# Kernel optimization log

Measured on AMD Instinct MI355X. Metric: run time of the kernel, lower is better.

The kernel has to match this reference:

```python
import jax, jax.numpy as jnp
import numpy as np

GRID_LO = 32
GRID_HI = 128
NF = 4          # n_features
K = 9           # num_neighbors
NUM_CLASSES = 36
BS = 128
P_LO = GRID_LO * GRID_LO   # 1024
P_HI = GRID_HI * GRID_HI   # 16384


def _knn_neighbor_indices():
    """Replicates cKDTree(lo_coords).query(hi_coords, k=K)[1]: lo grid has
    spacing ratio=grid_hi//grid_lo, hi grid spacing 1; neighbors sorted by
    distance (stable sort -> ties broken by lower linear index)."""
    ratio = GRID_HI // GRID_LO
    lo = np.stack(np.meshgrid(np.arange(GRID_LO) * ratio,
                              np.arange(GRID_LO) * ratio, indexing='ij'),
                  axis=-1).reshape(-1, 2).astype(np.float64)   # (P_LO, 2)
    hi = np.stack(np.meshgrid(np.arange(GRID_HI),
                              np.arange(GRID_HI), indexing='ij'),
                  axis=-1).reshape(-1, 2).astype(np.float64)   # (P_HI, 2)
    d2 = ((hi[:, None, :] - lo[None, :, :]) ** 2).sum(-1)      # (P_HI, P_LO)
    idx = np.argsort(d2, axis=1, kind='stable')[:, :K]          # (P_HI, K)
    return jnp.asarray(idx, dtype=jnp.int32)


def setup_inputs() -> dict:
    key = jax.random.key(0)
    k1, k2, k3, k4, k5 = jax.random.split(key, 5)
    x = jax.random.normal(k1, (BS, NF * P_LO), dtype=jnp.float32)
    cls_ids = jax.random.randint(k2, (BS,), 0, NUM_CLASSES)
    neighbor_indices = _knn_neighbor_indices()                  # (P_HI, K)
    weight_map = jax.random.normal(k3, (NUM_CLASSES, NF, P_HI, K), dtype=jnp.float32) * 0.05
    bias_low = jax.random.normal(k4, (NUM_CLASSES, NF, P_LO), dtype=jnp.float32) * 0.05
    bias_high = jax.random.normal(k5, (NUM_CLASSES, NF, P_HI), dtype=jnp.float32) * 0.05
    return {"x": x, "cls_ids": cls_ids, "neighbor_indices": neighbor_indices,
            "weight_map": weight_map, "bias_low": bias_low, "bias_high": bias_high}


def reference(x, cls_ids, neighbor_indices, weight_map, bias_low, bias_high):
    # x: (BS, NF*P_LO) -> (BS, NF, P_LO)
    y_low = x.reshape(x.shape[0], NF, P_LO)
    y_low_db = y_low - bias_low[cls_ids]                        # (BS, NF, P_LO)
    # gather k=9 lo-res neighbors for every hi-res pixel (all features at once)
    neigh = y_low_db[:, :, neighbor_indices]                    # (BS, NF, P_HI, K)
    weights = weight_map[cls_ids]                               # (BS, NF, P_HI, K)
    out = jnp.einsum('bfpk,bfpk->bfp', neigh, weights)          # weighted sum over k
    out = out + bias_high[cls_ids]                              # (BS, NF, P_HI)
    return out.reshape(x.shape[0], NF, GRID_HI, GRID_HI)
```

## Files before the change

### kernel.cpp

```cpp
#include <hip/hip_runtime.h>

#define BS      128
#define NF      4
#define NC      36
#define P_LO    1024
#define P_HI    16384
#define KNN     9
#define THREADS 256
#define TILE_P  256
#define NTILES  (P_HI / TILE_P)
#define LIST_OFF 64
#define SCHED_OFF 36

#define WBUF_BYTES (TILE_P * KNN * 4)
#define YBUF_BYTES (P_LO * 16)

__global__ __launch_bounds__(128) void build_lists_kernel(
    const int* __restrict__ cls_ids, int* __restrict__ ws)
{
    __shared__ int cnt[NC];
    __shared__ int pk[9];
    const int t = threadIdx.x;
    if (t < NC) cnt[t] = 0;
    if (t >= 64 && t < 73) pk[t - 64] = 0;
    __syncthreads();
    if (t < BS) {
        int c = cls_ids[t];
        int pos = atomicAdd(&cnt[c], 1);
        ws[LIST_OFF + c * BS + pos] = t;
    }
    __syncthreads();
    if (t < NC) {
        int ct = cnt[t];
        ws[t] = ct;
        int r = 0;
        for (int j = 0; j < NC; ++j) {
            int cj = cnt[j];
            r += (cj > ct) || (cj == ct && j < t);
        }
        atomicOr(&pk[r >> 2], t << ((r & 3) << 3));
    }
    __syncthreads();
    if (t < 9) ws[SCHED_OFF + t] = pk[t];
}

__device__ __forceinline__ void async_cp16(const void* g, void* l) {
    __builtin_amdgcn_global_load_lds(
        (const __attribute__((address_space(1))) void*)g,
        (__attribute__((address_space(3))) void*)l, 16, 0, 0);
}

__global__ __launch_bounds__(THREADS) void rect_up_kernel(
    const float* __restrict__ x,
    const int*   __restrict__ ws,
    const int*   __restrict__ nbr,
    const float* __restrict__ wmap,
    const float* __restrict__ blo,
    const float* __restrict__ bhi,
    float*       __restrict__ out)
{
    __shared__ __align__(16) char smem[WBUF_BYTES + YBUF_BYTES];

    const int tile = blockIdx.x & (NTILES - 1);
    const int g    = blockIdx.x >> 6;
    const int cls  = (ws[SCHED_OFF + (g >> 2)] >> ((g & 3) << 3)) & 0xFF;

    const int n_b = ws[cls];
    if (n_b == 0) return;

    const int tid   = threadIdx.x;
    const int tbase = tile * TILE_P;
    const int p     = tbase + tid;

    float4* wbuf  = (float4*)smem;
    float4* ybuf4 = (float4*)(smem + WBUF_BYTES);
    float4* idst  = ybuf4;

    {
        const float4* wsrc = (const float4*)(wmap + ((size_t)(cls * NF + 0) * P_HI + tbase) * KNN);
        const float4* isrc = (const float4*)(nbr + (size_t)tbase * KNN);
        async_cp16(wsrc + tid,       wbuf + tid);
        async_cp16(wsrc + tid + 256, wbuf + tid + 256);
        async_cp16(isrc + tid,       idst + tid);
        async_cp16(isrc + tid + 256, idst + tid + 256);
        if (tid < 64) {
            async_cp16(wsrc + 512 + tid, wbuf + 512 + tid);
            async_cp16(isrc + 512 + tid, idst + 512 + tid);
        }
    }

    const int* list = ws + LIST_OFF + cls * BS;
    const int bid0 = list[0];
    const int bid1 = (1 < n_b) ? list[1] : bid0;
    const int bid2 = (2 < n_b) ? list[2] : bid0;
    const int bid3 = (3 < n_b) ? list[3] : bid0;

    float xv[16];
    {
        const float* x0 = x + ((size_t)(bid0 * NF + 0)) * P_LO;
        const float* x1 = x + ((size_t)(bid1 * NF + 0)) * P_LO;
        const float* x2 = x + ((size_t)(bid2 * NF + 0)) * P_LO;
        const float* x3 = x + ((size_t)(bid3 * NF + 0)) * P_LO;
        #pragma unroll
        for (int m = 0; m < 4; ++m) {
            const int q = tid + (m << 8);
            xv[m * 4 + 0] = x0[q];
            xv[m * 4 + 1] = x1[q];
            xv[m * 4 + 2] = x2[q];
            xv[m * 4 + 3] = x3[q];
        }
    }

    asm volatile("s_waitcnt vmcnt(0)" ::: "memory");
    __syncthreads();

    int nb[KNN];
    {
        const int* irow = (const int*)(smem + WBUF_BYTES) + (size_t)tid * KNN;
        #pragma unroll
        for (int k = 0; k < KNN; ++k) nb[k] = irow[k];
    }

    const int R = (n_b + 3) >> 2;

    for (int f = 0; f < NF; ++f) {
        float blv[4];
        {
            const float* blp = blo + (size_t)(cls * NF + f) * P_LO;
            #pragma unroll
            for (int m = 0; m < 4; ++m) blv[m] = blp[tid + (m << 8)];
        }
        const float bh = bhi[(size_t)(cls * NF + f) * P_HI + p];

        float w[KNN];
        {
            const float* wrow = (const float*)smem + (size_t)tid * KNN;
            #pragma unroll
            for (int k = 0; k < KNN; ++k) w[k] = wrow[k];
        }
        __syncthreads();

        for (int r = 0; r < R; ++r) {
            int c0, c1, c2, c3;
            if (r == 0) {
                c0 = bid0; c1 = bid1; c2 = bid2; c3 = bid3;
                #pragma unroll
                for (int m = 0; m < 4; ++m) {
                    float4 v;
                    v.x = xv[m * 4 + 0] - blv[m];
                    v.y = xv[m * 4 + 1] - blv[m];
                    v.z = xv[m * 4 + 2] - blv[m];
                    v.w = xv[m * 4 + 3] - blv[m];
                    ybuf4[tid + (m << 8)] = v;
                }
            } else {
                const int s0 = 4 * r;
                c0 = list[s0];
                c1 = (s0 + 1 < n_b) ? list[s0 + 1] : c0;
                c2 = (s0 + 2 < n_b) ? list[s0 + 2] : c0;
                c3 = (s0 + 3 < n_b) ? list[s0 + 3] : c0;
                const float* x0 = x + ((size_t)(c0 * NF + f)) * P_LO;
                const float* x1 = x + ((size_t)(c1 * NF + f)) * P_LO;
                const float* x2 = x + ((size_t)(c2 * NF + f)) * P_LO;
                const float* x3 = x + ((size_t)(c3 * NF + f)) * P_LO;
                #pragma unroll
                for (int m = 0; m < 4; ++m) {
                    const int q = tid + (m << 8);
                    float4 v;
                    v.x = x0[q] - blv[m];
                    v.y = x1[q] - blv[m];
                    v.z = x2[q] - blv[m];
                    v.w = x3[q] - blv[m];
                    ybuf4[q] = v;
                }
            }
            __syncthreads();

            if (r == 0 && f + 1 < NF) {
                const float4* wsrc = (const float4*)(wmap + ((size_t)(cls * NF + f + 1) * P_HI + tbase) * KNN);
                async_cp16(wsrc + tid,       wbuf + tid);
                async_cp16(wsrc + tid + 256, wbuf + tid + 256);
                if (tid < 64) async_cp16(wsrc + 512 + tid, wbuf + 512 + tid);
                const float* x0 = x + ((size_t)(bid0 * NF + f + 1)) * P_LO;
                const float* x1 = x + ((size_t)(bid1 * NF + f + 1)) * P_LO;
                const float* x2 = x + ((size_t)(bid2 * NF + f + 1)) * P_LO;
                const float* x3 = x + ((size_t)(bid3 * NF + f + 1)) * P_LO;
                #pragma unroll
                for (int m = 0; m < 4; ++m) {
                    const int q = tid + (m << 8);
                    xv[m * 4 + 0] = x0[q];
                    xv[m * 4 + 1] = x1[q];
                    xv[m * 4 + 2] = x2[q];
                    xv[m * 4 + 3] = x3[q];
                }
            }

            float a0 = 0.f, a1 = 0.f, a2 = 0.f, a3 = 0.f;
            #pragma unroll
            for (int k = 0; k < KNN; ++k) {
                const float4 yv = ybuf4[nb[k]];
                a0 = fmaf(w[k], yv.x, a0);
                a1 = fmaf(w[k], yv.y, a1);
                a2 = fmaf(w[k], yv.z, a2);
                a3 = fmaf(w[k], yv.w, a3);
            }
            const int s0 = 4 * r;
            out[(size_t)(c0 * NF + f) * P_HI + p] = a0 + bh;
            if (s0 + 1 < n_b) out[(size_t)(c1 * NF + f) * P_HI + p] = a1 + bh;
            if (s0 + 2 < n_b) out[(size_t)(c2 * NF + f) * P_HI + p] = a2 + bh;
            if (s0 + 3 < n_b) out[(size_t)(c3 * NF + f) * P_HI + p] = a3 + bh;

            if (r + 1 < R) __syncthreads();
        }
        if (f + 1 < NF) __syncthreads();
    }
}

extern "C" void kernel_launch(void* const* d_in, const int* in_sizes, int n_in,
                              void* d_out, int out_size, void* d_ws, size_t ws_size,
                              hipStream_t stream) {
    const float* x    = (const float*)d_in[0];
    const int*   cls  = (const int*)d_in[1];
    const int*   nbr  = (const int*)d_in[2];
    const float* wmap = (const float*)d_in[3];
    const float* blo  = (const float*)d_in[4];
    const float* bhi  = (const float*)d_in[5];
    float*       out  = (float*)d_out;
    int*         wsl  = (int*)d_ws;

    build_lists_kernel<<<1, 128, 0, stream>>>(cls, wsl);
    rect_up_kernel<<<NC * NTILES, THREADS, 0, stream>>>(
        x, wsl, nbr, wmap, blo, bhi, out);
}
```

Baseline: 163.8 us.

## Split features across blocks and prefetch next batch group during compute

The grid grows so that each block handles a single feature instead of looping over all four. Weights and neighbor indices now come straight from global memory into registers, replacing the async LDS copies. Inside the batch-group loop, x for the next group is loaded into registers before the current gather runs, and barriers wait only on lgkmcnt rather than doing a full syncthreads. This gives four times more blocks for better occupancy and less serialization, at the cost of the neighbor indices being reloaded once per feature block.

New measurement: 159.4 us. 1.03x faster.

```diff
diff --git a/kernel.cpp b/kernel.cpp
--- a/kernel.cpp
+++ b/kernel.cpp
@@ -11,9 +11,6 @@
 #define NTILES  (P_HI / TILE_P)
 #define LIST_OFF 64
 #define SCHED_OFF 36
-
-#define WBUF_BYTES (TILE_P * KNN * 4)
-#define YBUF_BYTES (P_LO * 16)
 
 __global__ __launch_bounds__(128) void build_lists_kernel(
     const int* __restrict__ cls_ids, int* __restrict__ ws)
@@ -44,10 +41,9 @@
     if (t < 9) ws[SCHED_OFF + t] = pk[t];
 }
 
-__device__ __forceinline__ void async_cp16(const void* g, void* l) {
-    __builtin_amdgcn_global_load_lds(
-        (const __attribute__((address_space(1))) void*)g,
-        (__attribute__((address_space(3))) void*)l, 16, 0, 0);
+__device__ __forceinline__ void lds_barrier() {
+    asm volatile("s_waitcnt lgkmcnt(0)" ::: "memory");
+    __builtin_amdgcn_s_barrier();
 }
 
 __global__ __launch_bounds__(THREADS) void rect_up_kernel(
@@ -59,11 +55,14 @@
     const float* __restrict__ bhi,
     float*       __restrict__ out)
 {
-    __shared__ __align__(16) char smem[WBUF_BYTES + YBUF_BYTES];
+    __shared__ __align__(16) float4 ybuf4[P_LO];
+    __shared__ int ls[BS];
 
     const int tile = blockIdx.x & (NTILES - 1);
     const int g    = blockIdx.x >> 6;
-    const int cls  = (ws[SCHED_OFF + (g >> 2)] >> ((g & 3) << 3)) & 0xFF;
+    const int f    = g & (NF - 1);
+    const int rank = g >> 2;
+    const int cls  = (ws[SCHED_OFF + (rank >> 2)] >> ((rank & 3) << 3)) & 0xFF;
 
     const int n_b = ws[cls];
     if (n_b == 0) return;
@@ -72,35 +71,35 @@
     const int tbase = tile * TILE_P;
     const int p     = tbase + tid;
 
-    float4* wbuf  = (float4*)smem;
-    float4* ybuf4 = (float4*)(smem + WBUF_BYTES);
-    float4* idst  = ybuf4;
+    const int* list = ws + LIST_OFF + cls * BS;
+    if (tid < n_b) ls[tid] = list[tid];
 
+    int c0 = list[0];
+    int c1 = (1 < n_b) ? list[1] : c0;
+    int c2 = (2 < n_b) ? list[2] : c0;
+    int c3 = (3 < n_b) ? list[3] : c0;
+
+    float w[KNN]; int nb[KNN];
     {
-        const float4* wsrc = (const float4*)(wmap + ((size_t)(cls * NF + 0) * P_HI + tbase) * KNN);
-        const float4* isrc = (const float4*)(nbr + (size_t)tbase * KNN);
-        async_cp16(wsrc + tid,       wbuf + tid);
-        async_cp16(wsrc + tid + 256, wbuf + tid + 256);
-        async_cp16(isrc + tid,       idst + tid);
-        async_cp16(isrc + tid + 256, idst + tid + 256);
-        if (tid < 64) {
-            async_cp16(wsrc + 512 + tid, wbuf + 512 + tid);
-            async_cp16(isrc + 512 + tid, idst + 512 + tid);
-        }
+        const float* wr = wmap + ((size_t)(cls * NF + f) * P_HI + p) * KNN;
+        const int*   ir = nbr + (size_t)p * KNN;
+        #pragma unroll
+        for (int k = 0; k < KNN; ++k) { w[k] = wr[k]; nb[k] = ir[k]; }
     }
-
-    const int* list = ws + LIST_OFF + cls * BS;
-    const int bid0 = list[0];
-    const int bid1 = (1 < n_b) ? list[1] : bid0;
-    const int bid2 = (2 < n_b) ? list[2] : bid0;
-    const int bid3 = (3 < n_b) ? list[3] : bid0;
+    float blv[4];
+    {
+        const float* blp = blo + (size_t)(cls * NF + f) * P_LO;
+        #pragma unroll
+        for (int m = 0; m < 4; ++m) blv[m] = blp[tid + (m << 8)];
+    }
+    const float bh = bhi[(size_t)(cls * NF + f) * P_HI + p];
 
     float xv[16];
     {
-        const float* x0 = x + ((size_t)(bid0 * NF + 0)) * P_LO;
-        const float* x1 = x + ((size_t)(bid1 * NF + 0)) * P_LO;
-        const float* x2 = x + ((size_t)(bid2 * NF + 0)) * P_LO;
-        const float* x3 = x + ((size_t)(bid3 * NF + 0)) * P_LO;
+        const float* x0 = x + (size_t)(c0 * NF + f) * P_LO;
+        const float* x1 = x + (size_t)(c1 * NF + f) * P_LO;
+        const float* x2 = x + (size_t)(c2 * NF + f) * P_LO;
+        const float* x3 = x + (size_t)(c3 * NF + f) * P_LO;
         #pragma unroll
         for (int m = 0; m < 4; ++m) {
             const int q = tid + (m << 8);
@@ -111,108 +110,60 @@
         }
     }
 
-    asm volatile("s_waitcnt vmcnt(0)" ::: "memory");
-    __syncthreads();
-
-    int nb[KNN];
-    {
-        const int* irow = (const int*)(smem + WBUF_BYTES) + (size_t)tid * KNN;
-        #pragma unroll
-        for (int k = 0; k < KNN; ++k) nb[k] = irow[k];
-    }
-
     const int R = (n_b + 3) >> 2;
 
-    for (int f = 0; f < NF; ++f) {
-        float blv[4];
-        {
-            const float* blp = blo + (size_t)(cls * NF + f) * P_LO;
+    for (int r = 0; r < R; ++r) {
+        #pragma unroll
+        for (int m = 0; m < 4; ++m) {
+            const int q = tid + (m << 8);
+            float4 v;
+            v.x = xv[m * 4 + 0] - blv[m];
+            v.y = xv[m * 4 + 1] - blv[m];
+            v.z = xv[m * 4 + 2] - blv[m];
+            v.w = xv[m * 4 + 3] - blv[m];
+            ybuf4[q] = v;
+        }
+        lds_barrier();
+
+        const int s0 = 4 * r;
+        const int d0 = c0, d1 = c1, d2 = c2, d3 = c3;
+
+        if (r + 1 < R) {
+            const int s = s0 + 4;
+            c0 = ls[s];
+            c1 = (s + 1 < n_b) ? ls[s + 1] : c0;
+            c2 = (s + 2 < n_b) ? ls[s + 2] : c0;
+            c3 = (s + 3 < n_b) ? ls[s + 3] : c0;
+            const float* x0 = x + (size_t)(c0 * NF + f) * P_LO;
+            const float* x1 = x + (size_t)(c1 * NF + f) * P_LO;
+            const float* x2 = x + (size_t)(c2 * NF + f) * P_LO;
+            const float* x3 = x + (size_t)(c3 * NF + f) * P_LO;
             #pragma unroll
-            for (int m = 0; m < 4; ++m) blv[m] = blp[tid + (m << 8)];
+            for (int m = 0; m < 4; ++m) {
+                const int q = tid + (m << 8);
+                xv[m * 4 + 0] = x0[q];
+                xv[m * 4 + 1] = x1[q];
+                xv[m * 4 + 2] = x2[q];
+                xv[m * 4 + 3] = x3[q];
+            }
         }
-        const float bh = bhi[(size_t)(cls * NF + f) * P_HI + p];
 
-        float w[KNN];
-        {
-            const float* wrow = (const float*)smem + (size_t)tid * KNN;
-            #pragma unroll
-            for (int k = 0; k < KNN; ++k) w[k] = wrow[k];
+        float a0 = 0.f, a1 = 0.f, a2 = 0.f, a3 = 0.f;
+        #pragma unroll
+        for (int k = 0; k < KNN; ++k) {
+            const float4 yv = ybuf4[nb[k]];
+            a0 = fmaf(w[k], yv.x, a0);
+            a1 = fmaf(w[k], yv.y, a1);
+            a2 = fmaf(w[k], yv.z, a2);
+            a3 = fmaf(w[k], yv.w, a3);
         }
-        __syncthreads();
 
-        for (int r = 0; r < R; ++r) {
-            int c0, c1, c2, c3;
-            if (r == 0) {
-                c0 = bid0; c1 = bid1; c2 = bid2; c3 = bid3;
-                #pragma unroll
-                for (int m = 0; m < 4; ++m) {
-                    float4 v;
-                    v.x = xv[m * 4 + 0] - blv[m];
-                    v.y = xv[m * 4 + 1] - blv[m];
-                    v.z = xv[m * 4 + 2] - blv[m];
-                    v.w = xv[m * 4 + 3] - blv[m];
-                    ybuf4[tid + (m << 8)] = v;
-                }
-            } else {
-                const int s0 = 4 * r;
-                c0 = list[s0];
-                c1 = (s0 + 1 < n_b) ? list[s0 + 1] : c0;
-                c2 = (s0 + 2 < n_b) ? list[s0 + 2] : c0;
-                c3 = (s0 + 3 < n_b) ? list[s0 + 3] : c0;
-                const float* x0 = x + ((size_t)(c0 * NF + f)) * P_LO;
-                const float* x1 = x + ((size_t)(c1 * NF + f)) * P_LO;
-                const float* x2 = x + ((size_t)(c2 * NF + f)) * P_LO;
-                const float* x3 = x + ((size_t)(c3 * NF + f)) * P_LO;
-                #pragma unroll
-                for (int m = 0; m < 4; ++m) {
-                    const int q = tid + (m << 8);
-                    float4 v;
-                    v.x = x0[q] - blv[m];
-                    v.y = x1[q] - blv[m];
-                    v.z = x2[q] - blv[m];
-                    v.w = x3[q] - blv[m];
-                    ybuf4[q] = v;
-                }
-            }
-            __syncthreads();
+        out[(size_t)(d0 * NF + f) * P_HI + p] = a0 + bh;
+        if (s0 + 1 < n_b) out[(size_t)(d1 * NF + f) * P_HI + p] = a1 + bh;
+        if (s0 + 2 < n_b) out[(size_t)(d2 * NF + f) * P_HI + p] = a2 + bh;
+        if (s0 + 3 < n_b) out[(size_t)(d3 * NF + f) * P_HI + p] = a3 + bh;
 
-            if (r == 0 && f + 1 < NF) {
-                const float4* wsrc = (const float4*)(wmap + ((size_t)(cls * NF + f + 1) * P_HI + tbase) * KNN);
-                async_cp16(wsrc + tid,       wbuf + tid);
-                async_cp16(wsrc + tid + 256, wbuf + tid + 256);
-                if (tid < 64) async_cp16(wsrc + 512 + tid, wbuf + 512 + tid);
-                const float* x0 = x + ((size_t)(bid0 * NF + f + 1)) * P_LO;
-                const float* x1 = x + ((size_t)(bid1 * NF + f + 1)) * P_LO;
-                const float* x2 = x + ((size_t)(bid2 * NF + f + 1)) * P_LO;
-                const float* x3 = x + ((size_t)(bid3 * NF + f + 1)) * P_LO;
-                #pragma unroll
-                for (int m = 0; m < 4; ++m) {
-                    const int q = tid + (m << 8);
-                    xv[m * 4 + 0] = x0[q];
-                    xv[m * 4 + 1] = x1[q];
-                    xv[m * 4 + 2] = x2[q];
-                    xv[m * 4 + 3] = x3[q];
-                }
-            }
-
-            float a0 = 0.f, a1 = 0.f, a2 = 0.f, a3 = 0.f;
-            #pragma unroll
-            for (int k = 0; k < KNN; ++k) {
-                const float4 yv = ybuf4[nb[k]];
-                a0 = fmaf(w[k], yv.x, a0);
-                a1 = fmaf(w[k], yv.y, a1);
-                a2 = fmaf(w[k], yv.z, a2);
-                a3 = fmaf(w[k], yv.w, a3);
-            }
-            const int s0 = 4 * r;
-            out[(size_t)(c0 * NF + f) * P_HI + p] = a0 + bh;
-            if (s0 + 1 < n_b) out[(size_t)(c1 * NF + f) * P_HI + p] = a1 + bh;
-            if (s0 + 2 < n_b) out[(size_t)(c2 * NF + f) * P_HI + p] = a2 + bh;
-            if (s0 + 3 < n_b) out[(size_t)(c3 * NF + f) * P_HI + p] = a3 + bh;
-
-            if (r + 1 < R) __syncthreads();
-        }
-        if (f + 1 < NF) __syncthreads();
+        if (r + 1 < R) lds_barrier();
     }
 }
 
@@ -229,6 +180,6 @@
     int*         wsl  = (int*)d_ws;
 
     build_lists_kernel<<<1, 128, 0, stream>>>(cls, wsl);
-    rect_up_kernel<<<NC * NTILES, THREADS, 0, stream>>>(
+    rect_up_kernel<<<NC * NF * NTILES, THREADS, 0, stream>>>(
         x, wsl, nbr, wmap, blo, bhi, out);
 }
```
